# Performance work log

Measured on AMD Instinct MI355X. Metric: run time of the kernel, lower is better.

The kernel has to match this reference:

```python
import jax, jax.numpy as jnp
import numpy as np

B, T, D, H = 2, 2048, 1024, 16
DH = D // H


def setup_inputs() -> dict:
    key = jax.random.key(0)
    ks = jax.random.split(key, 5)
    scale = 1.0 / np.sqrt(D)
    return {
        "x": jax.random.normal(ks[0], (B, T, D), dtype=jnp.float32),
        "Wq": jax.random.normal(ks[1], (D, D), dtype=jnp.float32) * scale,
        "Wk": jax.random.normal(ks[2], (D, D), dtype=jnp.float32) * scale,
        "Wv": jax.random.normal(ks[3], (D, D), dtype=jnp.float32) * scale,
        "Wo": jax.random.normal(ks[4], (D, D), dtype=jnp.float32) * scale,
    }


def _split(y):
    # (B,T,D) -> (B,H,T,DH)
    b, t, _ = y.shape
    return y.reshape(b, t, H, DH).transpose(0, 2, 1, 3)


def reference(x, Wq, Wk, Wv, Wo):
    q = _split(x @ Wq)
    k = _split(x @ Wk)
    v = _split(x @ Wv)
    scores = jnp.einsum("bhqd,bhkd->bhqk", q, k) / jnp.sqrt(jnp.float32(DH))
    t = x.shape[1]
    # additive causal mask: -1e9 above the diagonal (matches band_part logic)
    causal = jnp.tril(jnp.ones((t, t), dtype=jnp.float32))
    scores = scores + (1.0 - causal) * -1e9
    attn = jax.nn.softmax(scores, axis=-1)
    out = jnp.einsum("bhqk,bhkd->bhqd", attn, v)  # (B,H,T,DH)
    out = out.transpose(0, 2, 1, 3).reshape(x.shape[0], t, D)
    return out @ Wo
```

## Files before the change

kernel.cpp:

```cpp
#include <hip/hip_runtime.h>

#define BB 2
#define TT 2048
#define DD 1024
#define HH 16
#define DHD 64
#define MM (BB*TT)

typedef __attribute__((ext_vector_type(8))) short short8;
typedef __attribute__((ext_vector_type(4))) float float4v;
typedef __attribute__((ext_vector_type(16))) float f32x16;
typedef unsigned short u16;

__device__ inline float bf2f(u16 u) {
    union { unsigned int i; float f; } v;
    v.i = ((unsigned int)u) << 16;
    return v.f;
}
__device__ inline u16 f2bf(float f) {
    union { float f; unsigned int i; } v;
    v.f = f;
    unsigned int x = v.i;
    unsigned int r = (x + 0x7fffu + ((x >> 16) & 1u)) >> 16;
    return (u16)r;
}
__device__ inline unsigned packtr(float x, float y) {
    union { float f; unsigned u; } a, b;
    a.f = x; b.f = y;
    return (a.u >> 16) | (b.u & 0xffff0000u);
}

__device__ inline void gl_lds16(const u16* g, u16* l) {
    __builtin_amdgcn_global_load_lds(
        (const __attribute__((address_space(1))) unsigned int*)g,
        (__attribute__((address_space(3))) unsigned int*)l, 16, 0, 0);
}

__global__ __launch_bounds__(256) void prep_k(const float* __restrict__ x,
                                              const float* __restrict__ Wq,
                                              const float* __restrict__ Wk,
                                              const float* __restrict__ Wv,
                                              const float* __restrict__ Wo,
                                              u16* __restrict__ xb,
                                              u16* __restrict__ WT) {
    int tid = threadIdx.x;
    if (blockIdx.z == 4) {
        int bid = blockIdx.y * 32 + blockIdx.x;
#pragma unroll
        for (int k = 0; k < 4; k++) {
            int i = bid * 1024 + k * 256 + tid;
            float4v v = ((const float4v*)x)[i];
            ushort4 o;
            o.x = f2bf(v[0]); o.y = f2bf(v[1]); o.z = f2bf(v[2]); o.w = f2bf(v[3]);
            ((ushort4*)xb)[i] = o;
        }
        return;
    }
    __shared__ u16 t[32][33];
    int wsel = blockIdx.z;
    const float* W = (wsel == 0) ? Wq : (wsel == 1) ? Wk : (wsel == 2) ? Wv : Wo;
    u16* o = WT + (size_t)wsel * DD * DD;
    int k0 = blockIdx.y * 32, n0 = blockIdx.x * 32;
    int tx = tid & 31, ty = tid >> 5;
#pragma unroll
    for (int i = 0; i < 4; i++) {
        int k = ty + i * 8;
        t[k][tx] = f2bf(W[(size_t)(k0 + k) * DD + n0 + tx]);
    }
    __syncthreads();
#pragma unroll
    for (int i = 0; i < 4; i++) {
        int n = ty + i * 8;
        o[(size_t)(n0 + n) * DD + k0 + tx] = t[tx][n];
    }
}

template <int MODE, int TM, int TN, int BK>
__global__ __launch_bounds__(256) void gemm_k(const u16* __restrict__ A,
                                              const u16* __restrict__ WT0,
                                              void* __restrict__ outp) {
    const int K = DD;
    const int MT = TM / 32, NT = TN / 32;
    const int NS = (TM + TN) * (BK / 8) / 256;
    const int CPR = BK / 8;

    int z = blockIdx.z;
    const u16* WT = WT0 + (size_t)z * DD * DD;
    int n0 = blockIdx.x * TN, m0 = blockIdx.y * TM;

    __shared__ u16 S[(TM + TN) * BK];

    int tid = threadIdx.x;
    int lane = tid & 63, w = tid >> 6;
    int wm = (w >> 1) * (TM / 2), wn = (w & 1) * (TN / 2);
    int quad = lane >> 4, l16 = lane & 15;

    const u16* gp[NS];
    u16* lp[NS];
#pragma unroll
    for (int j = 0; j < NS; j++) {
        int cid = tid + j * 256;
        int r = cid / CPR, c = cid % CPR;
        lp[j] = S + (size_t)cid * 8;
        gp[j] = (r < TM ? A + (size_t)(m0 + r) * K
                        : WT + (size_t)(n0 + r - TM) * K) + ((c ^ (r & 7)) * 8);
    }
    int swz = l16 & 7;

    float4v acc[MT][NT];
#pragma unroll
    for (int i = 0; i < MT; i++)
#pragma unroll
        for (int j = 0; j < NT; j++) acc[i][j] = (float4v)(0.0f);

    const int NK = K / BK;
#pragma unroll 1
    for (int ki = 0; ki < NK; ki++) {
        __syncthreads();
#pragma unroll
        for (int j = 0; j < NS; j++)
            gl_lds16(gp[j] + ki * BK, lp[j]);
        __syncthreads();

#pragma unroll
        for (int ks = 0; ks < BK / 32; ks++) {
            int cq = ((ks * 4 + quad) ^ swz) * 8;
            short8 a[MT], b[NT];
#pragma unroll
            for (int mt = 0; mt < MT; mt++)
                a[mt] = *(const short8*)&S[(wm + mt * 16 + l16) * BK + cq];
#pragma unroll
            for (int nt = 0; nt < NT; nt++)
                b[nt] = *(const short8*)&S[(TM + wn + nt * 16 + l16) * BK + cq];
#pragma unroll
            for (int mt = 0; mt < MT; mt++)
#pragma unroll
                for (int nt = 0; nt < NT; nt++)
                    acc[mt][nt] = __builtin_amdgcn_mfma_f32_16x16x32_bf16(
                        a[mt], b[nt], acc[mt][nt], 0, 0, 0);
        }
    }

#pragma unroll
    for (int mt = 0; mt < MT; mt++) {
#pragma unroll
        for (int nt = 0; nt < NT; nt++) {
#pragma unroll
            for (int r = 0; r < 4; r++) {
                int m = m0 + wm + mt * 16 + quad * 4 + r;
                int n = n0 + wn + nt * 16 + l16;
                float v = acc[mt][nt][r];
                if constexpr (MODE == 0) {
                    int bb = m >> 11, t = m & 2047;
                    int h = n >> 6, dh = n & 63;
                    size_t idx;
                    if (z == 2)
                        idx = (((size_t)2 * BB * HH + bb * HH + h) * DHD + dh) * TT + t;
                    else
                        idx = (((size_t)z * BB * HH + bb * HH + h) * TT + t) * DHD + dh;
                    ((u16*)outp)[idx] = f2bf(v);
                } else {
                    ((float*)outp)[(size_t)m * DD + n] = v;
                }
            }
        }
    }
}

__global__ __launch_bounds__(512, 2) void attn_k(const u16* __restrict__ QKV,
                                                 u16* __restrict__ AO) {
    const u16* Q  = QKV;
    const u16* Kp = QKV + (size_t)MM * DD;
    const u16* Vp = QKV + (size_t)2 * MM * DD;
    int bx = blockIdx.x, by = blockIdx.y;
    int bh = bx;
    int t_ = by & 7, s_ = by >> 3;
    int qt = ((bx ^ s_) & 1) ? (15 - t_) : t_;
    size_t hoff = (size_t)bh * TT * DHD;

    __shared__ u16 Ks[2][2][64 * 64];
    __shared__ u16 VTs[2][2][64 * 64];

    int tid = threadIdx.x;
    int lane = tid & 63, wv = tid >> 6;
    int g = wv >> 2, w4 = wv & 3;
    int l31 = lane & 31, hi = lane >> 5;
    int swz = l31 & 7;

    int sr = tid >> 3, sc = tid & 7;
    int sl = sr * 64 + ((sc ^ (sr & 7)) * 8);
    const u16* gK = Kp + hoff + (size_t)sr * DHD + sc * 8;
    const u16* gV = Vp + hoff + (size_t)sr * TT + sc * 8;

    const float qscale = 0.125f * 1.4426950408889634f;
    int q0 = qt * 128;
    short8 qB[4];
    {
        const u16* gq = Q + hoff + (size_t)(q0 + w4 * 32 + l31) * DHD + hi * 8;
#pragma unroll
        for (int kt = 0; kt < 4; kt++) {
            short8 v = *(const short8*)(gq + 16 * kt);
            short8 sv;
#pragma unroll
            for (int e = 0; e < 8; e++) sv[e] = (short)f2bf(bf2f((u16)v[e]) * qscale);
            qB[kt] = sv;
        }
    }

    short8 prK[2], prV[2];
    prK[0] = *(const short8*)gK;
    prK[1] = *(const short8*)(gK + (size_t)64 * DHD);
    prV[0] = *(const short8*)gV;
    prV[1] = *(const short8*)(gV + 64);

    const int NR = qt + 1;

    f32x16 o0 = (f32x16)(0.0f), o1 = (f32x16)(0.0f);
    float lr = 0.0f;

#pragma unroll 1
    for (int jt = 0; jt < NR; jt++) {
        int db = jt & 1;
#pragma unroll
        for (int tt = 0; tt < 2; tt++) {
            *(short8*)&Ks[db][tt][sl]  = prK[tt];
            *(short8*)&VTs[db][tt][sl] = prV[tt];
        }
        __syncthreads();

        if (jt + 1 < NR) {
            size_t nj = (size_t)(jt + 1) * 128;
            prK[0] = *(const short8*)(gK + nj * DHD);
            prK[1] = *(const short8*)(gK + (nj + 64) * DHD);
            prV[0] = *(const short8*)(gV + nj);
            prV[1] = *(const short8*)(gV + nj + 64);
        }

        f32x16 s0 = (f32x16)(0.0f), s1 = (f32x16)(0.0f);
#pragma unroll
        for (int kt = 0; kt < 4; kt++) {
            int ch = ((hi + 2 * kt) ^ swz) * 8;
            short8 ak0 = *(const short8*)&Ks[db][g][l31 * 64 + ch];
            short8 ak1 = *(const short8*)&Ks[db][g][(32 + l31) * 64 + ch];
            s0 = __builtin_amdgcn_mfma_f32_32x32x16_bf16(ak0, qB[kt], s0, 0, 0, 0);
            s1 = __builtin_amdgcn_mfma_f32_32x32x16_bf16(ak1, qB[kt], s1, 0, 0, 0);
        }

        if (jt == qt) {
            int lim = w4 * 32 + l31 - g * 64;
#pragma unroll
            for (int r = 0; r < 16; r++) {
                int kvl = (r & 3) + 8 * (r >> 2) + 4 * hi;
                if (kvl > lim) s0[r] = -30000.0f;
                if (32 + kvl > lim) s1[r] = -30000.0f;
            }
        }

#pragma unroll
        for (int r = 0; r < 16; r++) {
            s0[r] = __builtin_amdgcn_exp2f(s0[r]);
            s1[r] = __builtin_amdgcn_exp2f(s1[r]);
            lr += s0[r] + s1[r];
        }

        short8 pa[4];
#pragma unroll
        for (int kt2 = 0; kt2 < 4; kt2++) {
            f32x16 ps = (kt2 < 2) ? s0 : s1;
            const int base = 8 * (kt2 & 1);
            float e0 = ps[base + 0], e1 = ps[base + 1];
            float e2 = ps[base + 2], e3 = ps[base + 3];
            float e4 = ps[base + 4], e5 = ps[base + 5];
            float e6 = ps[base + 6], e7 = ps[base + 7];
            unsigned lA = packtr(e0, e1), lB = packtr(e2, e3);
            unsigned hA = packtr(e4, e5), hB = packtr(e6, e7);
            unsigned wA = hi ? hA : lA, wB = hi ? hB : lB;
            unsigned sA = hi ? lA : hA, sB = hi ? lB : hB;
            unsigned rA = (unsigned)__shfl_xor((int)sA, 32);
            unsigned rB = (unsigned)__shfl_xor((int)sB, 32);
            union { unsigned w[4]; short8 v; } u;
            u.w[0] = hi ? rA : wA; u.w[1] = hi ? rB : wB;
            u.w[2] = hi ? wA : rA; u.w[3] = hi ? wB : rB;
            pa[kt2] = u.v;
        }

#pragma unroll
        for (int kt2 = 0; kt2 < 4; kt2++) {
            int ch = ((hi + 2 * kt2) ^ swz) * 8;
            short8 bv0 = *(const short8*)&VTs[db][g][l31 * 64 + ch];
            short8 bv1 = *(const short8*)&VTs[db][g][(32 + l31) * 64 + ch];
            o0 = __builtin_amdgcn_mfma_f32_32x32x16_bf16(pa[kt2], bv0, o0, 0, 0, 0);
            o1 = __builtin_amdgcn_mfma_f32_32x32x16_bf16(pa[kt2], bv1, o1, 0, 0, 0);
        }
    }

    __syncthreads();
    float* Of = (float*)&Ks[0][0][0];
    float* Lf = (float*)&VTs[0][0][0];
    if (g == 1) {
#pragma unroll
        for (int r = 0; r < 16; r++) {
            Of[((w4 * 2 + 0) * 16 + r) * 64 + lane] = o0[r];
            Of[((w4 * 2 + 1) * 16 + r) * 64 + lane] = o1[r];
        }
        Lf[w4 * 64 + lane] = lr;
    }
    __syncthreads();
    if (g == 0) {
#pragma unroll
        for (int r = 0; r < 16; r++) {
            o0[r] += Of[((w4 * 2 + 0) * 16 + r) * 64 + lane];
            o1[r] += Of[((w4 * 2 + 1) * 16 + r) * 64 + lane];
        }
        lr += Lf[w4 * 64 + lane];

        float rs = lr + __shfl_xor(lr, 32);

        int b = bh >> 4, h = bh & 15;
#pragma unroll
        for (int r = 0; r < 16; r++) {
            int qlc = (r & 3) + 8 * (r >> 2) + 4 * hi;
            float ri = 1.0f / __shfl(rs, qlc);
            int q = q0 + w4 * 32 + qlc;
            size_t rb = (size_t)(b * TT + q) * DD + h * 64 + l31;
            AO[rb]      = f2bf(o0[r] * ri);
            AO[rb + 32] = f2bf(o1[r] * ri);
        }
    }
}

extern "C" void kernel_launch(void* const* d_in, const int* in_sizes, int n_in,
                              void* d_out, int out_size, void* d_ws, size_t ws_size,
                              hipStream_t stream) {
    const float* x  = (const float*)d_in[0];
    const float* Wq = (const float*)d_in[1];
    const float* Wk = (const float*)d_in[2];
    const float* Wv = (const float*)d_in[3];
    const float* Wo = (const float*)d_in[4];

    u16* xb  = (u16*)d_ws;
    u16* WT  = xb + (size_t)MM * DD;
    u16* QKV = WT + (size_t)4 * DD * DD;
    u16* AO  = QKV + (size_t)3 * MM * DD;
    float* out = (float*)d_out;

    prep_k<<<dim3(32, 32, 5), 256, 0, stream>>>(x, Wq, Wk, Wv, Wo, xb, WT);
    gemm_k<0, 128, 128, 64><<<dim3(DD / 128, MM / 128, 3), 256, 0, stream>>>(xb, WT, QKV);
    attn_k<<<dim3(32, 16), 512, 0, stream>>>(QKV, AO);
    gemm_k<1, 64, 128, 64><<<dim3(DD / 128, MM / 64, 1), 256, 0, stream>>>(AO, WT + (size_t)3 * DD * DD, out);
}
```

Measured before the change: 171.8 us.

## Load V operands directly from global into registers, drop V shared staging

The V^T tile is no longer staged through double-buffered shared memory. Each lane now loads its MFMA B-operand fragments for V directly from global memory at the start of every KV iteration. This halves the attention kernel's LDS footprint, and the launch bounds are raised from 2 to 4 blocks per CU to use the freed space. The trade-off is redundant global V reads across the two wave groups, which are not prefetched a tile ahead, plus tighter register limits that may cause spills.

Result: slower. 229.1 us (+33.4%).

```diff
diff --git a/kernel.cpp b/kernel.cpp
--- a/kernel.cpp
+++ b/kernel.cpp
@@ -167,7 +167,7 @@
     }
 }
 
-__global__ __launch_bounds__(512, 2) void attn_k(const u16* __restrict__ QKV,
+__global__ __launch_bounds__(512, 4) void attn_k(const u16* __restrict__ QKV,
                                                  u16* __restrict__ AO) {
     const u16* Q  = QKV;
     const u16* Kp = QKV + (size_t)MM * DD;
@@ -179,7 +179,7 @@
     size_t hoff = (size_t)bh * TT * DHD;
 
     __shared__ u16 Ks[2][2][64 * 64];
-    __shared__ u16 VTs[2][2][64 * 64];
+    __shared__ float Lfs[4 * 64];
 
     int tid = threadIdx.x;
     int lane = tid & 63, wv = tid >> 6;
@@ -190,7 +190,9 @@
     int sr = tid >> 3, sc = tid & 7;
     int sl = sr * 64 + ((sc ^ (sr & 7)) * 8);
     const u16* gK = Kp + hoff + (size_t)sr * DHD + sc * 8;
-    const u16* gV = Vp + hoff + (size_t)sr * TT + sc * 8;
+
+    const u16* gv0 = Vp + hoff + (size_t)l31 * TT + (size_t)g * 64 + hi * 8;
+    const u16* gv1 = gv0 + (size_t)32 * TT;
 
     const float qscale = 0.125f * 1.4426950408889634f;
     int q0 = qt * 128;
@@ -207,11 +209,9 @@
         }
     }
 
-    short8 prK[2], prV[2];
+    short8 prK[2];
     prK[0] = *(const short8*)gK;
     prK[1] = *(const short8*)(gK + (size_t)64 * DHD);
-    prV[0] = *(const short8*)gV;
-    prV[1] = *(const short8*)(gV + 64);
 
     const int NR = qt + 1;
 
@@ -222,18 +222,25 @@
     for (int jt = 0; jt < NR; jt++) {
         int db = jt & 1;
 #pragma unroll
-        for (int tt = 0; tt < 2; tt++) {
-            *(short8*)&Ks[db][tt][sl]  = prK[tt];
-            *(short8*)&VTs[db][tt][sl] = prV[tt];
-        }
+        for (int tt = 0; tt < 2; tt++)
+            *(short8*)&Ks[db][tt][sl] = prK[tt];
         __syncthreads();
 
         if (jt + 1 < NR) {
             size_t nj = (size_t)(jt + 1) * 128;
             prK[0] = *(const short8*)(gK + nj * DHD);
             prK[1] = *(const short8*)(gK + (nj + 64) * DHD);
-            prV[0] = *(const short8*)(gV + nj);
-            prV[1] = *(const short8*)(gV + nj + 64);
+        }
+
+        short8 bvr0[4], bvr1[4];
+        {
+            const u16* v0 = gv0 + (size_t)jt * 128;
+            const u16* v1 = gv1 + (size_t)jt * 128;
+#pragma unroll
+            for (int kt2 = 0; kt2 < 4; kt2++) {
+                bvr0[kt2] = *(const short8*)(v0 + kt2 * 16);
+                bvr1[kt2] = *(const short8*)(v1 + kt2 * 16);
+            }
         }
 
         f32x16 s0 = (f32x16)(0.0f), s1 = (f32x16)(0.0f);
@@ -286,24 +293,20 @@
 
 #pragma unroll
         for (int kt2 = 0; kt2 < 4; kt2++) {
-            int ch = ((hi + 2 * kt2) ^ swz) * 8;
-            short8 bv0 = *(const short8*)&VTs[db][g][l31 * 64 + ch];
-            short8 bv1 = *(const short8*)&VTs[db][g][(32 + l31) * 64 + ch];
-            o0 = __builtin_amdgcn_mfma_f32_32x32x16_bf16(pa[kt2], bv0, o0, 0, 0, 0);
-            o1 = __builtin_amdgcn_mfma_f32_32x32x16_bf16(pa[kt2], bv1, o1, 0, 0, 0);
+            o0 = __builtin_amdgcn_mfma_f32_32x32x16_bf16(pa[kt2], bvr0[kt2], o0, 0, 0, 0);
+            o1 = __builtin_amdgcn_mfma_f32_32x32x16_bf16(pa[kt2], bvr1[kt2], o1, 0, 0, 0);
         }
     }
 
     __syncthreads();
     float* Of = (float*)&Ks[0][0][0];
-    float* Lf = (float*)&VTs[0][0][0];
     if (g == 1) {
 #pragma unroll
         for (int r = 0; r < 16; r++) {
             Of[((w4 * 2 + 0) * 16 + r) * 64 + lane] = o0[r];
             Of[((w4 * 2 + 1) * 16 + r) * 64 + lane] = o1[r];
         }
-        Lf[w4 * 64 + lane] = lr;
+        Lfs[w4 * 64 + lane] = lr;
     }
     __syncthreads();
     if (g == 0) {
@@ -312,7 +315,7 @@
             o0[r] += Of[((w4 * 2 + 0) * 16 + r) * 64 + lane];
             o1[r] += Of[((w4 * 2 + 1) * 16 + r) * 64 + lane];
         }
-        lr += Lf[w4 * 64 + lane];
+        lr += Lfs[w4 * 64 + lane];
 
         float rs = lr + __shfl_xor(lr, 32);
 
```
